# Kernel optimization log

Measured on AMD Instinct MI355X. Metric: run time of the kernel, lower is better.

Reference implementation:

```python
import jax, jax.numpy as jnp
import numpy as np

NEG_SLOPE = 0.2


def add_self_loops(edge_index, num_nodes):
    loop = jnp.arange(num_nodes, dtype=edge_index.dtype)
    src = jnp.concatenate([edge_index[0], loop])
    dst = jnp.concatenate([edge_index[1], loop])
    return src, dst


def gat_conv(x, src, dst, W, att_src, att_dst, bias, heads, out_ch, concat):
    N = x.shape[0]
    h = (x @ W).reshape(N, heads, out_ch)                      # [N,H,C]
    a_src = jnp.sum(h * att_src, axis=-1)                      # [N,H]
    a_dst = jnp.sum(h * att_dst, axis=-1)                      # [N,H]
    e = a_src[src] + a_dst[dst]                                # [E,H]
    e = jax.nn.leaky_relu(e, NEG_SLOPE)
    # segment softmax over incoming edges of each destination node
    m = jax.ops.segment_max(e, dst, num_segments=N)            # [N,H]
    m = jnp.where(jnp.isfinite(m), m, 0.0)
    ex = jnp.exp(e - m[dst])
    s = jax.ops.segment_sum(ex, dst, num_segments=N)           # [N,H]
    alpha = ex / jnp.where(s[dst] > 0, s[dst], 1.0)            # [E,H]
    msg = alpha[:, :, None] * h[src]                           # [E,H,C]
    out = jax.ops.segment_sum(msg, dst, num_segments=N)        # [N,H,C]
    if concat:
        out = out.reshape(N, heads * out_ch)
    else:
        out = out.mean(axis=1)
    return out + bias


def setup_inputs() -> dict:
    key = jax.random.key(0)
    ks = jax.random.split(key, 10)
    N, F, E, H, C1 = 50000, 128, 800000, 8, 8
    x = jax.random.normal(ks[0], (N, F), dtype=jnp.float32)
    edge_index = jax.random.randint(ks[1], (2, E), 0, N, dtype=jnp.int64)
    sc = 0.1
    W1 = jax.random.normal(ks[2], (F, H * C1), dtype=jnp.float32) * sc
    a_src1 = jax.random.normal(ks[3], (H, C1), dtype=jnp.float32) * sc
    a_dst1 = jax.random.normal(ks[4], (H, C1), dtype=jnp.float32) * sc
    b1 = jnp.zeros((H * C1,), dtype=jnp.float32)
    W2 = jax.random.normal(ks[5], (H * C1, F), dtype=jnp.float32) * sc
    a_src2 = jax.random.normal(ks[6], (1, F), dtype=jnp.float32) * sc
    a_dst2 = jax.random.normal(ks[7], (1, F), dtype=jnp.float32) * sc
    b2 = jnp.zeros((F,), dtype=jnp.float32)
    return {"x": x, "edge_index": edge_index, "W1": W1, "a_src1": a_src1,
            "a_dst1": a_dst1, "b1": b1, "W2": W2, "a_src2": a_src2,
            "a_dst2": a_dst2, "b2": b2}


def reference(x, edge_index, W1, a_src1, a_dst1, b1, W2, a_src2, a_dst2, b2):
    N = x.shape[0]
    src, dst = add_self_loops(edge_index, N)
    h = gat_conv(x, src, dst, W1, a_src1, a_dst1, b1, heads=8, out_ch=8, concat=True)
    h = jax.nn.elu(h)
    out = gat_conv(h, src, dst, W2, a_src2, a_dst2, b2, heads=1, out_ch=x.shape[1], concat=True)
    return out
```

## Files before the change

kernel.cpp:

```cpp
#include <hip/hip_runtime.h>
#include <hip/hip_fp16.h>
#include <math.h>

#define NEG_SLOPE 0.2f
#define BSTRIDE 6144
#define L2E 1.4426950408889634f

typedef _Float16 f16x8 __attribute__((ext_vector_type(8)));
typedef float    f32x4 __attribute__((ext_vector_type(4)));

__device__ __forceinline__ void get_edge(const int* __restrict__ ei, int E, int e,
                                         int& s, int& d) {
    if (e < E) { s = ei[e]; d = ei[E + e]; }
    else       { s = e - E; d = e - E; }
}

union G1SMem {
    unsigned int sWu[4096];
    struct {
        int lhist[256], lbase[256], lrank[256], gbase[256];
        unsigned int sbuf[4096];
        int saddr[4096];
    } sc;
};

__global__ __launch_bounds__(256) void g1s_kernel(const float* __restrict__ x,
                                                  const float* __restrict__ W,
                                                  const float* __restrict__ asrc,
                                                  const float* __restrict__ adst,
                                                  _Float16* __restrict__ hout,
                                                  float* __restrict__ av,
                                                  float* __restrict__ bv, int N,
                                                  int gblocks,
                                                  const float* __restrict__ W2,
                                                  const float* __restrict__ as2,
                                                  const float* __restrict__ ad2,
                                                  float* __restrict__ wa,
                                                  float* __restrict__ wb,
                                                  int* __restrict__ bcur,
                                                  const int* __restrict__ ei, int E, int ET,
                                                  unsigned int* __restrict__ bstore,
                                                  int nbuck) {
    __shared__ G1SMem sm;
    int t = threadIdx.x;

    if (blockIdx.x == (unsigned)gblocks) {
        if (t < 64) {
            const float* wr = W2 + t * 128;
            float sa = 0.f, sb = 0.f;
#pragma unroll 8
            for (int c = 0; c < 128; ++c) {
                float w = wr[c];
                sa = fmaf(w, as2[c], sa);
                sb = fmaf(w, ad2[c], sb);
            }
            wa[t] = sa * L2E; wb[t] = sb * L2E;
        }
        return;
    }

    if (blockIdx.x > (unsigned)gblocks) {
        int sblk = blockIdx.x - gblocks - 1;
        int start = sblk * 4096;
        int cnt = ET - start; if (cnt > 4096) cnt = 4096;
        sm.sc.lhist[t] = 0; sm.sc.lrank[t] = 0;
        __syncthreads();
        int mybuck[16]; unsigned int myval[16];
#pragma unroll
        for (int k = 0; k < 16; ++k) {
            int e = start + t + k * 256;
            mybuck[k] = -1;
            if (e < ET) {
                int s, d; get_edge(ei, E, e, s, d);
                mybuck[k] = d >> 8;
                myval[k] = ((unsigned int)d << 16) | (unsigned int)s;
                atomicAdd(&sm.sc.lhist[mybuck[k]], 1);
            }
        }
        __syncthreads();
        int v = sm.sc.lhist[t];
        sm.sc.lbase[t] = v;
        __syncthreads();
        for (int off = 1; off < 256; off <<= 1) {
            int u = (t >= off) ? sm.sc.lbase[t - off] : 0;
            __syncthreads();
            sm.sc.lbase[t] += u;
            __syncthreads();
        }
        int excl = sm.sc.lbase[t] - v;
        if (t < nbuck && v > 0)
            sm.sc.gbase[t] = t * BSTRIDE + atomicAdd(&bcur[t], v);
        __syncthreads();
        sm.sc.lbase[t] = excl;
        __syncthreads();
#pragma unroll
        for (int k = 0; k < 16; ++k) {
            int b = mybuck[k];
            if (b >= 0) {
                int r = atomicAdd(&sm.sc.lrank[b], 1);
                int idx = sm.sc.lbase[b] + r;
                sm.sc.sbuf[idx] = myval[k];
                sm.sc.saddr[idx] = sm.sc.gbase[b] + r;
            }
        }
        __syncthreads();
        for (int j = t; j < cnt; j += 256)
            bstore[sm.sc.saddr[j]] = sm.sc.sbuf[j];
        return;
    }

    for (int p = t; p < 4096; p += 256) {
        int frag = p >> 8;
        int lane = (p >> 2) & 63;
        int j2   = p & 3;
        int chunk = frag >> 2, nt = frag & 3;
        int k = chunk * 32 + ((lane >> 4) << 3) + (j2 << 1);
        int n = nt * 16 + (lane & 15);
        union { _Float16 h[2]; unsigned int u; } pk;
        pk.h[0] = (_Float16)W[k * 64 + n];
        pk.h[1] = (_Float16)W[(k + 1) * 64 + n];
        sm.sWu[p] = pk.u;
    }
    __syncthreads();

    int lane = t & 63;
    int wid  = t >> 6;
    int rbase = blockIdx.x * 64 + wid * 16;
    int l15 = lane & 15, quad = lane >> 4;
    int rA = rbase + l15; if (rA >= N) rA = N - 1;

    const unsigned int* fragbase = &sm.sWu[lane * 4];
    f32x4 z = {0.f, 0.f, 0.f, 0.f};
    f32x4 acc[4] = {z, z, z, z};

#pragma unroll
    for (int chunk = 0; chunk < 4; ++chunk) {
        const float* xp = x + (size_t)rA * 128 + chunk * 32 + quad * 8;
        float4 f0 = *((const float4*)xp);
        float4 f1 = *((const float4*)(xp + 4));
        f16x8 af;
        af[0] = (_Float16)f0.x; af[1] = (_Float16)f0.y;
        af[2] = (_Float16)f0.z; af[3] = (_Float16)f0.w;
        af[4] = (_Float16)f1.x; af[5] = (_Float16)f1.y;
        af[6] = (_Float16)f1.z; af[7] = (_Float16)f1.w;
#pragma unroll
        for (int tt = 0; tt < 4; ++tt) {
            f16x8 bf = *((const f16x8*)(fragbase + (chunk * 4 + tt) * 256));
            acc[tt] = __builtin_amdgcn_mfma_f32_16x16x32_f16(af, bf, acc[tt], 0, 0, 0);
        }
    }

    float asc[4], adc[4];
#pragma unroll
    for (int tt = 0; tt < 4; ++tt) {
        asc[tt] = asrc[tt * 16 + l15] * L2E;
        adc[tt] = adst[tt * 16 + l15] * L2E;
    }
#pragma unroll
    for (int reg = 0; reg < 4; ++reg) {
        int r = rbase + quad * 4 + reg;
        bool ok = (r < N);
#pragma unroll
        for (int tt = 0; tt < 4; ++tt) {
            float v = acc[tt][reg];
            if (ok) hout[(size_t)r * 64 + tt * 16 + l15] = (_Float16)v;
            float pa = v * asc[tt], pb = v * adc[tt];
            pa += __shfl_xor(pa, 1); pb += __shfl_xor(pb, 1);
            pa += __shfl_xor(pa, 2); pb += __shfl_xor(pb, 2);
            pa += __shfl_xor(pa, 4); pb += __shfl_xor(pb, 4);
            if (ok && (lane & 7) == 0) {
                int head = tt * 2 + (l15 >> 3);
                av[r * 8 + head] = pa;
                bv[r * 8 + head] = pb;
            }
        }
    }
}

__global__ __launch_bounds__(256) void bucket_csr64(const unsigned int* __restrict__ bstore,
                                                    const int* __restrict__ bcur,
                                                    int* __restrict__ cnt,
                                                    unsigned short* __restrict__ col, int N) {
    __shared__ int lrank[256];
    int b = blockIdx.x, t = threadIdx.x;
    int base = b * BSTRIDE;
    int nb = bcur[b]; if (nb > BSTRIDE) nb = BSTRIDE;
    lrank[t] = 0;
    __syncthreads();
    for (int i = t; i < nb; i += 256) {
        unsigned int pk = bstore[base + i];
        int local = (pk >> 16) & 255;
        int r = atomicAdd(&lrank[local], 1);
        if (r < 64) col[(((b << 8) + local) << 6) + r] = (unsigned short)(pk & 0xFFFFu);
    }
    __syncthreads();
    int node = (b << 8) + t;
    if (node < N) {
        int deg = lrank[t]; if (deg > 64) deg = 64;
        cnt[node] = deg;
    }
}

__global__ __launch_bounds__(512) void agg1_kernel(const int* __restrict__ cnt,
                                                   const unsigned short* __restrict__ col,
                                                   const float* __restrict__ av,
                                                   const float* __restrict__ bv,
                                                   const __half* __restrict__ h1,
                                                   const float* __restrict__ b1,
                                                   const float* __restrict__ wa,
                                                   const float* __restrict__ wb,
                                                   _Float16* __restrict__ out1,
                                                   float* __restrict__ av2,
                                                   float* __restrict__ bv2, int N) {
    int lane = threadIdx.x & 63;
    int node = blockIdx.x * 16 + (threadIdx.x >> 6) * 2 + (lane >> 5);
    bool valid = node < N;
    int nodeC = valid ? node : 0;
    int g  = (lane >> 3) & 3;
    int gl = lane & 7;
    const unsigned short* colp = col + ((size_t)nodeC << 6);
    int deg = cnt[nodeC];
    int last = deg - 1; if (last < 0) last = 0;
    float bd = bv[nodeC * 8 + gl];
    const uint4* hrow = (const uint4*)h1;

    uint4 z4 = {0u, 0u, 0u, 0u};
    int e = g;
    int c0 = colp[e      <= last ? e      : last];
    int c1 = colp[e + 4  <= last ? e + 4  : last];
    int c2 = colp[e + 8  <= last ? e + 8  : last];
    float av0 = 0.f, av1v = 0.f; uint4 h0 = z4, h1v = z4;
    if (e < deg)     { av0  = av[c0 * 8 + gl]; h0  = hrow[(size_t)c0 * 8 + gl]; }
    if (e + 4 < deg) { av1v = av[c1 * 8 + gl]; h1v = hrow[(size_t)c1 * 8 + gl]; }

    float s = 0.f, a0 = 0.f, a1 = 0.f, a2 = 0.f, a3 = 0.f,
          a4 = 0.f, a5 = 0.f, a6 = 0.f, a7 = 0.f;
    for (; e < deg; e += 4) {
        float av2v = 0.f; uint4 h2 = z4;
        if (e + 8 < deg) { av2v = av[c2 * 8 + gl]; h2 = hrow[(size_t)c2 * 8 + gl]; }
        int c3 = colp[e + 12 <= last ? e + 12 : last];
        float l = av0 + bd;
        l = l > 0.f ? l : NEG_SLOPE * l;
        float w = __builtin_amdgcn_exp2f(l);
        float2 f0 = __half22float2(*(const __half2*)&h0.x);
        float2 f1 = __half22float2(*(const __half2*)&h0.y);
        float2 f2 = __half22float2(*(const __half2*)&h0.z);
        float2 f3 = __half22float2(*(const __half2*)&h0.w);
        s += w;
        a0 = fmaf(w, f0.x, a0); a1 = fmaf(w, f0.y, a1);
        a2 = fmaf(w, f1.x, a2); a3 = fmaf(w, f1.y, a3);
        a4 = fmaf(w, f2.x, a4); a5 = fmaf(w, f2.y, a5);
        a6 = fmaf(w, f3.x, a6); a7 = fmaf(w, f3.y, a7);
        av0 = av1v; h0 = h1v; av1v = av2v; h1v = h2; c2 = c3;
    }
#pragma unroll
    for (int off = 8; off < 32; off <<= 1) {
        s  += __shfl_xor(s, off);
        a0 += __shfl_xor(a0, off); a1 += __shfl_xor(a1, off);
        a2 += __shfl_xor(a2, off); a3 += __shfl_xor(a3, off);
        a4 += __shfl_xor(a4, off); a5 += __shfl_xor(a5, off);
        a6 += __shfl_xor(a6, off); a7 += __shfl_xor(a7, off);
    }
    float inv = __builtin_amdgcn_rcpf(s);
    float4 bb0 = ((const float4*)b1)[gl * 2];
    float4 bb1 = ((const float4*)b1)[gl * 2 + 1];
    float v0 = a0 * inv + bb0.x, v1 = a1 * inv + bb0.y;
    float v2 = a2 * inv + bb0.z, v3 = a3 * inv + bb0.w;
    float v4 = a4 * inv + bb1.x, v5 = a5 * inv + bb1.y;
    float v6 = a6 * inv + bb1.z, v7 = a7 * inv + bb1.w;
    v0 = v0 > 0.f ? v0 : __expf(v0) - 1.f; v1 = v1 > 0.f ? v1 : __expf(v1) - 1.f;
    v2 = v2 > 0.f ? v2 : __expf(v2) - 1.f; v3 = v3 > 0.f ? v3 : __expf(v3) - 1.f;
    v4 = v4 > 0.f ? v4 : __expf(v4) - 1.f; v5 = v5 > 0.f ? v5 : __expf(v5) - 1.f;
    v6 = v6 > 0.f ? v6 : __expf(v6) - 1.f; v7 = v7 > 0.f ? v7 : __expf(v7) - 1.f;
    float4 wa0 = ((const float4*)wa)[gl * 2], wa1 = ((const float4*)wa)[gl * 2 + 1];
    float4 wb0 = ((const float4*)wb)[gl * 2], wb1 = ((const float4*)wb)[gl * 2 + 1];
    float pa = v0 * wa0.x + v1 * wa0.y + v2 * wa0.z + v3 * wa0.w
             + v4 * wa1.x + v5 * wa1.y + v6 * wa1.z + v7 * wa1.w;
    float pb = v0 * wb0.x + v1 * wb0.y + v2 * wb0.z + v3 * wb0.w
             + v4 * wb1.x + v5 * wb1.y + v6 * wb1.z + v7 * wb1.w;
    pa += __shfl_xor(pa, 1); pb += __shfl_xor(pb, 1);
    pa += __shfl_xor(pa, 2); pb += __shfl_xor(pb, 2);
    pa += __shfl_xor(pa, 4); pb += __shfl_xor(pb, 4);
    if (valid && (lane & 31) == 0) { av2[node] = pa; bv2[node] = pb; }
    if (valid && g == 0) {
        f16x8 o;
        o[0] = (_Float16)v0; o[1] = (_Float16)v1; o[2] = (_Float16)v2; o[3] = (_Float16)v3;
        o[4] = (_Float16)v4; o[5] = (_Float16)v5; o[6] = (_Float16)v6; o[7] = (_Float16)v7;
        ((f16x8*)out1)[(size_t)node * 8 + gl] = o;
    }
}

__global__ __launch_bounds__(512) void agg2g2_kernel(const int* __restrict__ cnt,
                                                     const unsigned short* __restrict__ col,
                                                     const float* __restrict__ av,
                                                     const float* __restrict__ bv,
                                                     const __half* __restrict__ out1,
                                                     const float* __restrict__ W,
                                                     const float* __restrict__ b2,
                                                     float* __restrict__ dout, int N) {
    __shared__ unsigned int sWu[4096];
    __shared__ _Float16 sAgg[64][72];
    int t = threadIdx.x;
    int lane = t & 63;
    int wid  = t >> 6;
    int rbase = blockIdx.x * 64;

    for (int p = t; p < 4096; p += 512) {
        int frag = p >> 8;
        int ln = (p >> 2) & 63;
        int j2 = p & 3;
        int chunk = frag >> 3, nt = frag & 7;
        int k = chunk * 32 + ((ln >> 4) << 3) + (j2 << 1);
        int n = nt * 16 + (ln & 15);
        union { _Float16 h[2]; unsigned int u; } pk;
        pk.h[0] = (_Float16)W[k * 128 + n];
        pk.h[1] = (_Float16)W[(k + 1) * 128 + n];
        sWu[p] = pk.u;
    }

    int g  = (lane >> 3) & 3;
    int gl = lane & 7;
    const uint4* hrow = (const uint4*)out1;
    uint4 z4 = {0u, 0u, 0u, 0u};
#pragma unroll 1
    for (int pass = 0; pass < 4; ++pass) {
        int nl = pass * 16 + wid * 2 + (lane >> 5);
        int node = rbase + nl;
        bool valid = node < N;
        int nodeC = valid ? node : 0;
        const unsigned short* colp = col + ((size_t)nodeC << 6);
        int deg = cnt[nodeC];
        int last = deg - 1; if (last < 0) last = 0;
        float bd = bv[nodeC];

        int e = g;
        int c0 = colp[e      <= last ? e      : last];
        int c1 = colp[e + 4  <= last ? e + 4  : last];
        int c2 = colp[e + 8  <= last ? e + 8  : last];
        float av0 = 0.f, av1v = 0.f; uint4 h0 = z4, h1v = z4;
        if (e < deg)     { av0  = av[c0]; h0  = hrow[(size_t)c0 * 8 + gl]; }
        if (e + 4 < deg) { av1v = av[c1]; h1v = hrow[(size_t)c1 * 8 + gl]; }

        float s = 0.f, a0 = 0.f, a1 = 0.f, a2 = 0.f, a3 = 0.f,
              a4 = 0.f, a5 = 0.f, a6 = 0.f, a7 = 0.f;
        for (; e < deg; e += 4) {
            float av2v = 0.f; uint4 h2 = z4;
            if (e + 8 < deg) { av2v = av[c2]; h2 = hrow[(size_t)c2 * 8 + gl]; }
            int c3 = colp[e + 12 <= last ? e + 12 : last];
            float l = av0 + bd;
            l = l > 0.f ? l : NEG_SLOPE * l;
            float w = __builtin_amdgcn_exp2f(l);
            float2 f0 = __half22float2(*(const __half2*)&h0.x);
            float2 f1 = __half22float2(*(const __half2*)&h0.y);
            float2 f2 = __half22float2(*(const __half2*)&h0.z);
            float2 f3 = __half22float2(*(const __half2*)&h0.w);
            s += w;
            a0 = fmaf(w, f0.x, a0); a1 = fmaf(w, f0.y, a1);
            a2 = fmaf(w, f1.x, a2); a3 = fmaf(w, f1.y, a3);
            a4 = fmaf(w, f2.x, a4); a5 = fmaf(w, f2.y, a5);
            a6 = fmaf(w, f3.x, a6); a7 = fmaf(w, f3.y, a7);
            av0 = av1v; h0 = h1v; av1v = av2v; h1v = h2; c2 = c3;
        }
#pragma unroll
        for (int off = 8; off < 32; off <<= 1) {
            s  += __shfl_xor(s, off);
            a0 += __shfl_xor(a0, off); a1 += __shfl_xor(a1, off);
            a2 += __shfl_xor(a2, off); a3 += __shfl_xor(a3, off);
            a4 += __shfl_xor(a4, off); a5 += __shfl_xor(a5, off);
            a6 += __shfl_xor(a6, off); a7 += __shfl_xor(a7, off);
        }
        if (g == 0) {
            float inv = __builtin_amdgcn_rcpf(s);
            f16x8 o;
            o[0] = (_Float16)(a0 * inv); o[1] = (_Float16)(a1 * inv);
            o[2] = (_Float16)(a2 * inv); o[3] = (_Float16)(a3 * inv);
            o[4] = (_Float16)(a4 * inv); o[5] = (_Float16)(a5 * inv);
            o[6] = (_Float16)(a6 * inv); o[7] = (_Float16)(a7 * inv);
            *((f16x8*)&sAgg[nl][gl * 8]) = o;
        }
    }
    __syncthreads();

    int rblk = (wid & 3) * 16;
    int chalf = wid >> 2;
    int l15 = lane & 15, quad = lane >> 4;

    const unsigned int* fragbase = &sWu[lane * 4];
    f32x4 z = {0.f, 0.f, 0.f, 0.f};
    f32x4 acc[4] = {z, z, z, z};

#pragma unroll
    for (int chunk = 0; chunk < 2; ++chunk) {
        f16x8 af = *((const f16x8*)&sAgg[rblk + l15][chunk * 32 + quad * 8]);
#pragma unroll
        for (int tt = 0; tt < 4; ++tt) {
            f16x8 bf = *((const f16x8*)(fragbase + (chunk * 8 + chalf * 4 + tt) * 256));
            acc[tt] = __builtin_amdgcn_mfma_f32_16x16x32_f16(af, bf, acc[tt], 0, 0, 0);
        }
    }

    float bcol[4];
#pragma unroll
    for (int tt = 0; tt < 4; ++tt) bcol[tt] = b2[chalf * 64 + tt * 16 + l15];
#pragma unroll
    for (int reg = 0; reg < 4; ++reg) {
        int r = rbase + rblk + quad * 4 + reg;
        if (r < N) {
#pragma unroll
            for (int tt = 0; tt < 4; ++tt)
                dout[(size_t)r * 128 + chalf * 64 + tt * 16 + l15] = acc[tt][reg] + bcol[tt];
        }
    }
}

extern "C" void kernel_launch(void* const* d_in, const int* in_sizes, int n_in,
                              void* d_out, int out_size, void* d_ws, size_t ws_size,
                              hipStream_t stream) {
    const float* x      = (const float*)d_in[0];
    const int*   ei     = (const int*)  d_in[1];
    const float* W1     = (const float*)d_in[2];
    const float* a_src1 = (const float*)d_in[3];
    const float* a_dst1 = (const float*)d_in[4];
    const float* b1     = (const float*)d_in[5];
    const float* W2     = (const float*)d_in[6];
    const float* a_src2 = (const float*)d_in[7];
    const float* a_dst2 = (const float*)d_in[8];
    const float* b2     = (const float*)d_in[9];
    float* dout = (float*)d_out;

    const int N  = in_sizes[0] / 128;
    const int E  = in_sizes[1] / 2;
    const int ET = E + N;
    const int NBUCK = (N + 255) >> 8;
    const int NBLKA = (ET + 4095) >> 12;

    char* wsb = (char*)d_ws;
    _Float16* h1     = (_Float16*)wsb; wsb += (size_t)N * 64 * 2;
    _Float16* out1   = (_Float16*)wsb; wsb += (size_t)N * 64 * 2;
    float* av1  = (float*)wsb; wsb += (size_t)N * 8 * 4;
    float* bv1  = (float*)wsb; wsb += (size_t)N * 8 * 4;
    float* av2  = (float*)wsb; wsb += (size_t)N * 4;
    float* bv2  = (float*)wsb; wsb += (size_t)N * 4;
    float* wa   = (float*)wsb; wsb += 64 * 4;
    float* wb   = (float*)wsb; wsb += 64 * 4;
    int* cnt    = (int*)wsb; wsb += (size_t)N * 4;
    unsigned short* col = (unsigned short*)wsb; wsb += (size_t)N * 64 * 2;
    unsigned int* bstore = (unsigned int*)wsb; wsb += (size_t)NBUCK * BSTRIDE * 4;
    int* bcur   = (int*)wsb; wsb += 256 * 4;

    const int gblocks = (N + 63) / 64;

    hipMemsetAsync(bcur, 0, 256 * sizeof(int), stream);

    g1s_kernel<<<gblocks + 1 + NBLKA, 256, 0, stream>>>(x, W1, a_src1, a_dst1, h1, av1, bv1, N,
                                                        gblocks, W2, a_src2, a_dst2, wa, wb,
                                                        bcur, ei, E, ET, bstore, NBUCK);

    bucket_csr64<<<NBUCK, 256, 0, stream>>>(bstore, bcur, cnt, col, N);

    agg1_kernel<<<(N + 15) / 16, 512, 0, stream>>>(cnt, col, av1, bv1,
                                                   (const __half*)h1, b1, wa, wb,
                                                   out1, av2, bv2, N);

    agg2g2_kernel<<<gblocks, 512, 0, stream>>>(cnt, col, av2, bv2,
                                               (const __half*)out1, W2, b2, dout, N);
}
```

Before: 174.7 us.

## Fuse bucket-to-CSR build into layer-1 aggregation using shared-memory adjacency

Removes the separate bucket_csr64 launch. Each aggregation block now builds the neighbor lists for its own 64 nodes in shared memory by scanning its 256-node bucket and keeping only the entries for its quarter. It aggregates straight from that shared-memory list and writes col/cnt back to global memory for the layer-2 kernel. This saves one launch plus the global round-trip of col for layer 1. In exchange, each bucket is read four times, blocks are fewer and larger, and the prefetch now loads clamped edges unconditionally.

```diff
diff --git a/kernel.cpp b/kernel.cpp
--- a/kernel.cpp
+++ b/kernel.cpp
@@ -177,116 +177,128 @@
     }
 }
 
-__global__ __launch_bounds__(256) void bucket_csr64(const unsigned int* __restrict__ bstore,
+__global__ __launch_bounds__(512) void agg1q_kernel(const unsigned int* __restrict__ bstore,
                                                     const int* __restrict__ bcur,
+                                                    const float* __restrict__ av,
+                                                    const float* __restrict__ bv,
+                                                    const __half* __restrict__ h1,
+                                                    const float* __restrict__ b1,
+                                                    const float* __restrict__ wa,
+                                                    const float* __restrict__ wb,
+                                                    _Float16* __restrict__ out1,
+                                                    float* __restrict__ av2,
+                                                    float* __restrict__ bv2,
                                                     int* __restrict__ cnt,
-                                                    unsigned short* __restrict__ col, int N) {
-    __shared__ int lrank[256];
-    int b = blockIdx.x, t = threadIdx.x;
-    int base = b * BSTRIDE;
+                                                    unsigned short* __restrict__ colg,
+                                                    int N) {
+    __shared__ unsigned short colL[64][64];
+    __shared__ int lrank[64];
+    int t = threadIdx.x;
+    int b = blockIdx.x >> 2, q = blockIdx.x & 3;
+    int nbase = blockIdx.x * 64;
+
+    if (t < 64) { lrank[t] = 0; colL[t][0] = 0; }
+    __syncthreads();
+
     int nb = bcur[b]; if (nb > BSTRIDE) nb = BSTRIDE;
-    lrank[t] = 0;
+    const unsigned int* seg = bstore + (size_t)b * BSTRIDE;
+    for (int i = t; i < nb; i += 512) {
+        unsigned int pk = seg[i];
+        int local = (pk >> 16) & 255;
+        if ((local >> 6) == q) {
+            int r = atomicAdd(&lrank[local & 63], 1);
+            if (r < 64) colL[local & 63][r] = (unsigned short)(pk & 0xFFFFu);
+        }
+    }
     __syncthreads();
-    for (int i = t; i < nb; i += 256) {
-        unsigned int pk = bstore[base + i];
-        int local = (pk >> 16) & 255;
-        int r = atomicAdd(&lrank[local], 1);
-        if (r < 64) col[(((b << 8) + local) << 6) + r] = (unsigned short)(pk & 0xFFFFu);
-    }
-    __syncthreads();
-    int node = (b << 8) + t;
-    if (node < N) {
-        int deg = lrank[t]; if (deg > 64) deg = 64;
-        cnt[node] = deg;
-    }
-}
-
-__global__ __launch_bounds__(512) void agg1_kernel(const int* __restrict__ cnt,
-                                                   const unsigned short* __restrict__ col,
-                                                   const float* __restrict__ av,
-                                                   const float* __restrict__ bv,
-                                                   const __half* __restrict__ h1,
-                                                   const float* __restrict__ b1,
-                                                   const float* __restrict__ wa,
-                                                   const float* __restrict__ wb,
-                                                   _Float16* __restrict__ out1,
-                                                   float* __restrict__ av2,
-                                                   float* __restrict__ bv2, int N) {
-    int lane = threadIdx.x & 63;
-    int node = blockIdx.x * 16 + (threadIdx.x >> 6) * 2 + (lane >> 5);
-    bool valid = node < N;
-    int nodeC = valid ? node : 0;
+
+    for (int i = t; i < 4096; i += 512)
+        colg[(size_t)blockIdx.x * 4096 + i] = colL[i >> 6][i & 63];
+    if (t < 64) {
+        int node = nbase + t;
+        if (node < N) { int d = lrank[t]; if (d > 64) d = 64; cnt[node] = d; }
+    }
+
+    int lane = t & 63, wid = t >> 6;
     int g  = (lane >> 3) & 3;
     int gl = lane & 7;
-    const unsigned short* colp = col + ((size_t)nodeC << 6);
-    int deg = cnt[nodeC];
-    int last = deg - 1; if (last < 0) last = 0;
-    float bd = bv[nodeC * 8 + gl];
     const uint4* hrow = (const uint4*)h1;
 
-    uint4 z4 = {0u, 0u, 0u, 0u};
-    int e = g;
-    int c0 = colp[e      <= last ? e      : last];
-    int c1 = colp[e + 4  <= last ? e + 4  : last];
-    int c2 = colp[e + 8  <= last ? e + 8  : last];
-    float av0 = 0.f, av1v = 0.f; uint4 h0 = z4, h1v = z4;
-    if (e < deg)     { av0  = av[c0 * 8 + gl]; h0  = hrow[(size_t)c0 * 8 + gl]; }
-    if (e + 4 < deg) { av1v = av[c1 * 8 + gl]; h1v = hrow[(size_t)c1 * 8 + gl]; }
-
-    float s = 0.f, a0 = 0.f, a1 = 0.f, a2 = 0.f, a3 = 0.f,
-          a4 = 0.f, a5 = 0.f, a6 = 0.f, a7 = 0.f;
-    for (; e < deg; e += 4) {
-        float av2v = 0.f; uint4 h2 = z4;
-        if (e + 8 < deg) { av2v = av[c2 * 8 + gl]; h2 = hrow[(size_t)c2 * 8 + gl]; }
-        int c3 = colp[e + 12 <= last ? e + 12 : last];
-        float l = av0 + bd;
-        l = l > 0.f ? l : NEG_SLOPE * l;
-        float w = __builtin_amdgcn_exp2f(l);
-        float2 f0 = __half22float2(*(const __half2*)&h0.x);
-        float2 f1 = __half22float2(*(const __half2*)&h0.y);
-        float2 f2 = __half22float2(*(const __half2*)&h0.z);
-        float2 f3 = __half22float2(*(const __half2*)&h0.w);
-        s += w;
-        a0 = fmaf(w, f0.x, a0); a1 = fmaf(w, f0.y, a1);
-        a2 = fmaf(w, f1.x, a2); a3 = fmaf(w, f1.y, a3);
-        a4 = fmaf(w, f2.x, a4); a5 = fmaf(w, f2.y, a5);
-        a6 = fmaf(w, f3.x, a6); a7 = fmaf(w, f3.y, a7);
-        av0 = av1v; h0 = h1v; av1v = av2v; h1v = h2; c2 = c3;
-    }
-#pragma unroll
-    for (int off = 8; off < 32; off <<= 1) {
-        s  += __shfl_xor(s, off);
-        a0 += __shfl_xor(a0, off); a1 += __shfl_xor(a1, off);
-        a2 += __shfl_xor(a2, off); a3 += __shfl_xor(a3, off);
-        a4 += __shfl_xor(a4, off); a5 += __shfl_xor(a5, off);
-        a6 += __shfl_xor(a6, off); a7 += __shfl_xor(a7, off);
-    }
-    float inv = __builtin_amdgcn_rcpf(s);
-    float4 bb0 = ((const float4*)b1)[gl * 2];
-    float4 bb1 = ((const float4*)b1)[gl * 2 + 1];
-    float v0 = a0 * inv + bb0.x, v1 = a1 * inv + bb0.y;
-    float v2 = a2 * inv + bb0.z, v3 = a3 * inv + bb0.w;
-    float v4 = a4 * inv + bb1.x, v5 = a5 * inv + bb1.y;
-    float v6 = a6 * inv + bb1.z, v7 = a7 * inv + bb1.w;
-    v0 = v0 > 0.f ? v0 : __expf(v0) - 1.f; v1 = v1 > 0.f ? v1 : __expf(v1) - 1.f;
-    v2 = v2 > 0.f ? v2 : __expf(v2) - 1.f; v3 = v3 > 0.f ? v3 : __expf(v3) - 1.f;
-    v4 = v4 > 0.f ? v4 : __expf(v4) - 1.f; v5 = v5 > 0.f ? v5 : __expf(v5) - 1.f;
-    v6 = v6 > 0.f ? v6 : __expf(v6) - 1.f; v7 = v7 > 0.f ? v7 : __expf(v7) - 1.f;
-    float4 wa0 = ((const float4*)wa)[gl * 2], wa1 = ((const float4*)wa)[gl * 2 + 1];
-    float4 wb0 = ((const float4*)wb)[gl * 2], wb1 = ((const float4*)wb)[gl * 2 + 1];
-    float pa = v0 * wa0.x + v1 * wa0.y + v2 * wa0.z + v3 * wa0.w
-             + v4 * wa1.x + v5 * wa1.y + v6 * wa1.z + v7 * wa1.w;
-    float pb = v0 * wb0.x + v1 * wb0.y + v2 * wb0.z + v3 * wb0.w
-             + v4 * wb1.x + v5 * wb1.y + v6 * wb1.z + v7 * wb1.w;
-    pa += __shfl_xor(pa, 1); pb += __shfl_xor(pb, 1);
-    pa += __shfl_xor(pa, 2); pb += __shfl_xor(pb, 2);
-    pa += __shfl_xor(pa, 4); pb += __shfl_xor(pb, 4);
-    if (valid && (lane & 31) == 0) { av2[node] = pa; bv2[node] = pb; }
-    if (valid && g == 0) {
-        f16x8 o;
-        o[0] = (_Float16)v0; o[1] = (_Float16)v1; o[2] = (_Float16)v2; o[3] = (_Float16)v3;
-        o[4] = (_Float16)v4; o[5] = (_Float16)v5; o[6] = (_Float16)v6; o[7] = (_Float16)v7;
-        ((f16x8*)out1)[(size_t)node * 8 + gl] = o;
+#pragma unroll 1
+    for (int pass = 0; pass < 4; ++pass) {
+        int nl = pass * 16 + wid * 2 + (lane >> 5);
+        int node = nbase + nl;
+        bool valid = node < N;
+        int nodeC = valid ? node : 0;
+        int deg = lrank[nl]; if (deg > 64) deg = 64;
+        int last = deg - 1; if (last < 0) last = 0;
+        float bd = bv[nodeC * 8 + gl];
+
+        int e = g;
+        int m0 = e     <= last ? e     : last;
+        int m1 = e + 4 <= last ? e + 4 : last;
+        int m2 = e + 8 <= last ? e + 8 : last;
+        int c0 = colL[nl][m0], c1 = colL[nl][m1], c2 = colL[nl][m2];
+        float av0  = av[c0 * 8 + gl]; uint4 h0  = hrow[(size_t)c0 * 8 + gl];
+        float av1v = av[c1 * 8 + gl]; uint4 h1v = hrow[(size_t)c1 * 8 + gl];
+        float av2v = av[c2 * 8 + gl]; uint4 h2v = hrow[(size_t)c2 * 8 + gl];
+
+        float s = 0.f, a0 = 0.f, a1 = 0.f, a2 = 0.f, a3 = 0.f,
+              a4 = 0.f, a5 = 0.f, a6 = 0.f, a7 = 0.f;
+        for (; e < deg; e += 4) {
+            int m3 = e + 12 <= last ? e + 12 : last;
+            int c3 = colL[nl][m3];
+            float av3 = av[c3 * 8 + gl];
+            uint4 h3  = hrow[(size_t)c3 * 8 + gl];
+            float l = av0 + bd;
+            l = l > 0.f ? l : NEG_SLOPE * l;
+            float w = __builtin_amdgcn_exp2f(l);
+            float2 f0 = __half22float2(*(const __half2*)&h0.x);
+            float2 f1 = __half22float2(*(const __half2*)&h0.y);
+            float2 f2 = __half22float2(*(const __half2*)&h0.z);
+            float2 f3 = __half22float2(*(const __half2*)&h0.w);
+            s += w;
+            a0 = fmaf(w, f0.x, a0); a1 = fmaf(w, f0.y, a1);
+            a2 = fmaf(w, f1.x, a2); a3 = fmaf(w, f1.y, a3);
+            a4 = fmaf(w, f2.x, a4); a5 = fmaf(w, f2.y, a5);
+            a6 = fmaf(w, f3.x, a6); a7 = fmaf(w, f3.y, a7);
+            av0 = av1v; h0 = h1v; av1v = av2v; h1v = h2v; av2v = av3; h2v = h3;
+        }
+#pragma unroll
+        for (int off = 8; off < 32; off <<= 1) {
+            s  += __shfl_xor(s, off);
+            a0 += __shfl_xor(a0, off); a1 += __shfl_xor(a1, off);
+            a2 += __shfl_xor(a2, off); a3 += __shfl_xor(a3, off);
+            a4 += __shfl_xor(a4, off); a5 += __shfl_xor(a5, off);
+            a6 += __shfl_xor(a6, off); a7 += __shfl_xor(a7, off);
+        }
+        float inv = s > 0.f ? __builtin_amdgcn_rcpf(s) : 0.f;
+        float4 bb0 = ((const float4*)b1)[gl * 2];
+        float4 bb1 = ((const float4*)b1)[gl * 2 + 1];
+        float v0 = a0 * inv + bb0.x, v1 = a1 * inv + bb0.y;
+        float v2 = a2 * inv + bb0.z, v3 = a3 * inv + bb0.w;
+        float v4 = a4 * inv + bb1.x, v5 = a5 * inv + bb1.y;
+        float v6 = a6 * inv + bb1.z, v7 = a7 * inv + bb1.w;
+        v0 = v0 > 0.f ? v0 : __expf(v0) - 1.f; v1 = v1 > 0.f ? v1 : __expf(v1) - 1.f;
+        v2 = v2 > 0.f ? v2 : __expf(v2) - 1.f; v3 = v3 > 0.f ? v3 : __expf(v3) - 1.f;
+        v4 = v4 > 0.f ? v4 : __expf(v4) - 1.f; v5 = v5 > 0.f ? v5 : __expf(v5) - 1.f;
+        v6 = v6 > 0.f ? v6 : __expf(v6) - 1.f; v7 = v7 > 0.f ? v7 : __expf(v7) - 1.f;
+        float4 wa0 = ((const float4*)wa)[gl * 2], wa1 = ((const float4*)wa)[gl * 2 + 1];
+        float4 wb0 = ((const float4*)wb)[gl * 2], wb1 = ((const float4*)wb)[gl * 2 + 1];
+        float pa = v0 * wa0.x + v1 * wa0.y + v2 * wa0.z + v3 * wa0.w
+                 + v4 * wa1.x + v5 * wa1.y + v6 * wa1.z + v7 * wa1.w;
+        float pb = v0 * wb0.x + v1 * wb0.y + v2 * wb0.z + v3 * wb0.w
+                 + v4 * wb1.x + v5 * wb1.y + v6 * wb1.z + v7 * wb1.w;
+        pa += __shfl_xor(pa, 1); pb += __shfl_xor(pb, 1);
+        pa += __shfl_xor(pa, 2); pb += __shfl_xor(pb, 2);
+        pa += __shfl_xor(pa, 4); pb += __shfl_xor(pb, 4);
+        if (valid && (lane & 31) == 0) { av2[node] = pa; bv2[node] = pb; }
+        if (valid && g == 0) {
+            f16x8 o;
+            o[0] = (_Float16)v0; o[1] = (_Float16)v1; o[2] = (_Float16)v2; o[3] = (_Float16)v3;
+            o[4] = (_Float16)v4; o[5] = (_Float16)v5; o[6] = (_Float16)v6; o[7] = (_Float16)v7;
+            ((f16x8*)out1)[(size_t)node * 8 + gl] = o;
+        }
     }
 }
 
@@ -433,6 +445,7 @@
     const int ET = E + N;
     const int NBUCK = (N + 255) >> 8;
     const int NBLKA = (ET + 4095) >> 12;
+    const int NQ    = NBUCK * 4;
 
     char* wsb = (char*)d_ws;
     _Float16* h1     = (_Float16*)wsb; wsb += (size_t)N * 64 * 2;
@@ -444,7 +457,7 @@
     float* wa   = (float*)wsb; wsb += 64 * 4;
     float* wb   = (float*)wsb; wsb += 64 * 4;
     int* cnt    = (int*)wsb; wsb += (size_t)N * 4;
-    unsigned short* col = (unsigned short*)wsb; wsb += (size_t)N * 64 * 2;
+    unsigned short* col = (unsigned short*)wsb; wsb += (size_t)NQ * 4096 * 2;
     unsigned int* bstore = (unsigned int*)wsb; wsb += (size_t)NBUCK * BSTRIDE * 4;
     int* bcur   = (int*)wsb; wsb += 256 * 4;
 
@@ -456,11 +469,9 @@
                                                         gblocks, W2, a_src2, a_dst2, wa, wb,
                                                         bcur, ei, E, ET, bstore, NBUCK);
 
-    bucket_csr64<<<NBUCK, 256, 0, stream>>>(bstore, bcur, cnt, col, N);
-
-    agg1_kernel<<<(N + 15) / 16, 512, 0, stream>>>(cnt, col, av1, bv1,
-                                                   (const __half*)h1, b1, wa, wb,
-                                                   out1, av2, bv2, N);
+    agg1q_kernel<<<NQ, 512, 0, stream>>>(bstore, bcur, av1, bv1,
+                                         (const __half*)h1, b1, wa, wb,
+                                         out1, av2, bv2, cnt, col, N);
 
     agg2g2_kernel<<<gblocks, 512, 0, stream>>>(cnt, col, av2, bv2,
                                                (const __half*)out1, W2, b2, dout, N);
```

Measured after the change: 174.8 us. About the same (+0.1%).
